# Kernel optimization log

Hardware: AMD Instinct MI355X
Metric: run time of the kernel (lower is better)

Reference implementation:

```python
import jax, jax.numpy as jnp
import numpy as np
from jax import lax

T = 256          # sentence length
WD, TD = 300, 100  # word/tag embedding dims
H = WD + TD      # LSTM hidden (=input) size, per module __init__
VOCAB, NTAGS = 50000, 50
MLP_H = 400


def setup_inputs() -> dict:
    key = jax.random.key(0)
    ks = jax.random.split(key, 20)
    s = 0.05  # small init scale for numerical stability
    return {
        "words": jax.random.randint(ks[0], (T,), 0, VOCAB),
        "tags": jax.random.randint(ks[1], (T,), 0, NTAGS),
        "word_emb": jax.random.normal(ks[2], (VOCAB, WD), jnp.float32),
        "tag_emb": jax.random.normal(ks[3], (NTAGS, TD), jnp.float32),
        "Wih0": jax.random.normal(ks[4], (2, 4 * H, H), jnp.float32) * s,
        "Whh0": jax.random.normal(ks[5], (2, 4 * H, H), jnp.float32) * s,
        "bih0": jax.random.normal(ks[6], (2, 4 * H), jnp.float32) * s,
        "bhh0": jax.random.normal(ks[7], (2, 4 * H), jnp.float32) * s,
        "Wih1": jax.random.normal(ks[8], (2, 4 * H, 2 * H), jnp.float32) * s,
        "Whh1": jax.random.normal(ks[9], (2, 4 * H, H), jnp.float32) * s,
        "bih1": jax.random.normal(ks[10], (2, 4 * H), jnp.float32) * s,
        "bhh1": jax.random.normal(ks[11], (2, 4 * H), jnp.float32) * s,
        "W1": jax.random.normal(ks[12], (MLP_H, 4 * H), jnp.float32) * s,
        "b1": jax.random.normal(ks[13], (MLP_H,), jnp.float32) * s,
        "W2": jax.random.normal(ks[14], (1, MLP_H), jnp.float32) * s,
        "b2": jax.random.normal(ks[15], (1,), jnp.float32) * s,
        "h0": jax.random.normal(ks[16], (2, 2, H), jnp.float32),  # [layer, dir, H]
        "c0": jax.random.normal(ks[17], (2, 2, H), jnp.float32),
    }


def _lstm_dir(xs, Wih, Whh, bih, bhh, h0, c0, reverse):
    # xs: [T, D]; torch LSTM gate order i, f, g, o
    def step(carry, xt):
        h, c = carry
        g = xt @ Wih.T + bih + h @ Whh.T + bhh  # [4H]
        i, f, gg, o = jnp.split(g, 4)
        c = jax.nn.sigmoid(f) * c + jax.nn.sigmoid(i) * jnp.tanh(gg)
        h = jax.nn.sigmoid(o) * jnp.tanh(c)
        return (h, c), h
    _, hs = lax.scan(step, (h0, c0), xs, reverse=reverse)
    return hs  # [T, H]


def _forward(words, tags, word_emb, tag_emb, Wih0, Whh0, bih0, bhh0,
             Wih1, Whh1, bih1, bhh1, W1, b1, W2, b2, h0, c0):
    x = jnp.concatenate([word_emb[words], tag_emb[tags]], axis=1)  # [T, H]
    # layer 0, both directions
    hf0 = _lstm_dir(x, Wih0[0], Whh0[0], bih0[0], bhh0[0], h0[0, 0], c0[0, 0], False)
    hb0 = _lstm_dir(x, Wih0[1], Whh0[1], bih0[1], bhh0[1], h0[0, 1], c0[0, 1], True)
    x1 = jnp.concatenate([hf0, hb0], axis=1)  # [T, 2H]
    # layer 1
    hf1 = _lstm_dir(x1, Wih1[0], Whh1[0], bih1[0], bhh1[0], h0[1, 0], c0[1, 0], False)
    hb1 = _lstm_dir(x1, Wih1[1], Whh1[1], bih1[1], bhh1[1], h0[1, 1], c0[1, 1], True)
    hvec = jnp.concatenate([hf1, hb1], axis=1)  # [T, 2H]
    # batched pairwise MLP: score(i,j) = W2 @ tanh(W1 @ [h_i; h_j] + b1) + b2
    # Split W1 so the concat is never materialized over all T^2 pairs.
    W1a, W1b = W1[:, :2 * H], W1[:, 2 * H:]
    pi = hvec @ W1a.T  # [T, MLP_H] contribution of head word i
    pj = hvec @ W1b.T  # [T, MLP_H] contribution of dependent word j
    act = jnp.tanh(pi[:, None, :] + pj[None, :, :] + b1)  # [T, T, MLP_H]
    scores = act @ W2[0] + b2[0]  # [T, T]
    # diagonal stays 0 (permutations exclude i == j; scoreTensor was zeroed)
    return scores * (1.0 - jnp.eye(T, dtype=scores.dtype))


def reference(words, tags, word_emb, tag_emb, Wih0, Whh0, bih0, bhh0,
              Wih1, Whh1, bih1, bhh1, W1, b1, W2, b2, h0, c0):
    return _forward(words, tags, word_emb, tag_emb, Wih0, Whh0, bih0, bhh0,
                    Wih1, Whh1, bih1, bhh1, W1, b1, W2, b2, h0, c0)
```

## Files before the change

kernel.cpp:

```cpp
#include <hip/hip_runtime.h>
#include <hip/hip_bf16.h>

#define T 256
#define H 400
#define G4 1600
#define WD 300
#define TD 100
#define MLP_H 400
#define NBLK_D 25
#define HB 16
#define GR 64
#define WSTR 202
#define NPAIR 200

typedef _Float16 f16;
typedef _Float16 half2t __attribute__((ext_vector_type(2)));
typedef unsigned long long u64;
typedef unsigned int u32;

__device__ __forceinline__ float fexp(float x) {
    return __builtin_amdgcn_exp2f(x * 1.4426950408889634f);
}
__device__ __forceinline__ float sigf(float x) {
    return __builtin_amdgcn_rcpf(1.0f + fexp(-x));
}
__device__ __forceinline__ float tanhf_fast(float x) {
    return 1.0f - 2.0f * __builtin_amdgcn_rcpf(1.0f + fexp(2.0f * x));
}
__device__ __forceinline__ unsigned short f16bits(f16 x) {
    union { f16 h; unsigned short u; } v; v.h = x; return v.u;
}
__device__ __forceinline__ u32 packh2(float a, float b) {
    half2t hv; hv.x = (_Float16)a; hv.y = (_Float16)b;
    return __builtin_bit_cast(u32, hv);
}

#if __has_builtin(__builtin_amdgcn_fdot2)
__device__ __forceinline__ float dot2u(u32 a, u32 b, float c) {
    return __builtin_amdgcn_fdot2(__builtin_bit_cast(half2t, a),
                                  __builtin_bit_cast(half2t, b), c, false);
}
#else
__device__ __forceinline__ float dot2u(u32 a, u32 b, float c) {
    half2t x = __builtin_bit_cast(half2t, a), y = __builtin_bit_cast(half2t, b);
    return fmaf((float)x.y, (float)y.y, fmaf((float)x.x, (float)y.x, c));
}
#endif

__device__ __forceinline__ u64 sysload(const u64* p) {
    return __hip_atomic_load(p, __ATOMIC_RELAXED, __HIP_MEMORY_SCOPE_SYSTEM);
}
__device__ __forceinline__ void sysstore(u64* p, u64 v) {
    __hip_atomic_store(p, v, __ATOMIC_RELAXED, __HIP_MEMORY_SCOPE_SYSTEM);
}

__global__ void gather_k(const int* __restrict__ words, const int* __restrict__ tags,
                         const float* __restrict__ wemb, const float* __restrict__ temb,
                         float* __restrict__ x0) {
    int t = blockIdx.x;
    int w = words[t], g = tags[t];
    for (int c = threadIdx.x; c < H; c += 128) {
        float v = (c < WD) ? wemb[w * WD + c] : temb[g * TD + (c - WD)];
        x0[t * H + c] = v;
    }
}

__global__ __launch_bounds__(256) void gemm_tn(
    const float* __restrict__ X, int ldx,
    const float* __restrict__ Wt, int ldw, int wofs,
    const float* __restrict__ bias1, const float* __restrict__ bias2,
    float* __restrict__ out, int ldo, int Rt, int K) {
    __shared__ float Xs[64][17];
    __shared__ float Ws[64][17];
    const int tid = threadIdx.x;
    const int t0 = blockIdx.x * 64, r0 = blockIdx.y * 64;
    const int lr = tid >> 2, kq = (tid & 3) * 4;
    const int ti = tid >> 4, rj = tid & 15;
    float acc[4][4] = {};
    for (int k0 = 0; k0 < K; k0 += 16) {
        float4 xv = *(const float4*)(X + (size_t)(t0 + lr) * ldx + k0 + kq);
        Xs[lr][kq + 0] = xv.x; Xs[lr][kq + 1] = xv.y;
        Xs[lr][kq + 2] = xv.z; Xs[lr][kq + 3] = xv.w;
        int r = r0 + lr;
        float4 wv = make_float4(0.f, 0.f, 0.f, 0.f);
        if (r < Rt) wv = *(const float4*)(Wt + (size_t)r * ldw + wofs + k0 + kq);
        Ws[lr][kq + 0] = wv.x; Ws[lr][kq + 1] = wv.y;
        Ws[lr][kq + 2] = wv.z; Ws[lr][kq + 3] = wv.w;
        __syncthreads();
#pragma unroll
        for (int k = 0; k < 16; k++) {
            float xr[4], wr[4];
#pragma unroll
            for (int m = 0; m < 4; m++) xr[m] = Xs[ti * 4 + m][k];
#pragma unroll
            for (int n = 0; n < 4; n++) wr[n] = Ws[rj * 4 + n][k];
#pragma unroll
            for (int m = 0; m < 4; m++)
#pragma unroll
                for (int n = 0; n < 4; n++)
                    acc[m][n] = fmaf(xr[m], wr[n], acc[m][n]);
        }
        __syncthreads();
    }
    int rq = r0 + rj * 4;
    if (rq < Rt) {
        float b[4];
#pragma unroll
        for (int n = 0; n < 4; n++) {
            int r = rq + n;
            b[n] = (bias1 ? bias1[r] : 0.f) + (bias2 ? bias2[r] : 0.f);
        }
#pragma unroll
        for (int m = 0; m < 4; m++) {
            int t = t0 + ti * 4 + m;
            float4 o;
            o.x = acc[m][0] + b[0]; o.y = acc[m][1] + b[1];
            o.z = acc[m][2] + b[2]; o.w = acc[m][3] + b[3];
            *(float4*)(out + (size_t)t * ldo + rq) = o;
        }
    }
}

__global__ void lstm_init5(const float* __restrict__ h0, u64* sA, u64* sB) {
    int tid = threadIdx.x;
    const int TOT = 2 * 2 * NPAIR;
    for (int i = tid; i < TOT; i += 256) { sA[i] = 0xFFFFULL; sB[i] = 0xFFFFULL; }
    __syncthreads();
    for (int p = tid; p < 2 * NPAIR; p += 256) {
        int d = p / NPAIR, pr = p - d * NPAIR;
        size_t off = (size_t)(d * 2 + 0) * NPAIR + pr;
        f16 a0 = (f16)h0[d * H + 2 * pr], b0 = (f16)h0[d * H + 2 * pr + 1];
        sA[off] = 0ULL | ((u64)f16bits(a0) << 16) | ((u64)f16bits(b0) << 32);
        f16 a1 = (f16)h0[2 * H + d * H + 2 * pr], b1 = (f16)h0[2 * H + d * H + 2 * pr + 1];
        sB[off] = 0ULL | ((u64)f16bits(a1) << 16) | ((u64)f16bits(b1) << 32);
    }
}

__global__ __launch_bounds__(512, 1) void lstm_layer8(
    const float* __restrict__ G,
    const float* __restrict__ Whh,
    const float* __restrict__ c0l,
    float* __restrict__ xout,
    u64* __restrict__ slots) {
    const int role = blockIdx.x;
    const int dir = role / NBLK_D, blk = role - dir * NBLK_D;
    const int tid = threadIdx.x;
    const float* Wd = Whh + (size_t)dir * G4 * H;
    const float* Gd = G + (size_t)dir * T * G4;
    u64* sd = slots + (size_t)dir * 2 * NPAIR;

    __shared__ u32 wlds[GR * WSTR];
    __shared__ __align__(16) u32 hsh[NPAIR];
    __shared__ float gsum[GR];
    __shared__ float gsh[2][GR];

    for (int idx = tid; idx < GR * 100; idx += 512) {
        int row = idx / 100, c4 = idx - row * 100;
        int g = row >> 4, r = row & 15;
        const float4* src = (const float4*)(Wd + (size_t)(g * H + blk * HB + r) * H);
        float4 f = src[c4];
        *(uint2*)&wlds[row * WSTR + c4 * 2] =
            make_uint2(packh2(f.x, f.y), packh2(f.z, f.w));
    }
    if (tid >= 448) {
        int i = tid - 448, gg = i >> 4, rr = i & 15;
        int tt0 = dir ? (T - 1) : 0;
        gsh[0][i] = Gd[(size_t)tt0 * G4 + gg * H + blk * HB + rr];
    } else if (tid < 8) {
        u64 v = sysload(sd + blk * 8 + tid);
        hsh[blk * 8 + tid] = (u32)(v >> 16);
    }
    float c = (tid < 64) ? c0l[dir * H + blk * HB + (tid & 15)] : 0.f;
    __syncthreads();

#pragma clang loop unroll(disable)
    for (int s = 0; s < T; ++s) {
        if (tid >= 256 && tid < 448) {
            int f = tid - 256;
            int widx = f + (f >= blk * 8 ? 8 : 0);
            u64* src = sd + (size_t)(s & 1) * NPAIR + widx;
            u64 v = sysload(src);
            int spins = 0;
            while ((unsigned)(v & 0xFFFFULL) != (unsigned)s) {
                if (++spins > 16384) {
                    v = __hip_atomic_fetch_add(src, 0ULL, __ATOMIC_RELAXED,
                                               __HIP_MEMORY_SCOPE_AGENT);
                } else {
                    v = sysload(src);
                }
            }
            hsh[widx] = (u32)(v >> 16);
        } else if (tid >= 448) {
            int sn = (s + 1 < T) ? (s + 1) : s;
            int tt = dir ? (T - 1 - sn) : sn;
            int i = tid - 448, gg = i >> 4, rr = i & 15;
            gsh[(s + 1) & 1][i] = Gd[(size_t)tt * G4 + gg * H + blk * HB + rr];
        }
        __syncthreads();

        if (tid < 256) {
            const int row = tid >> 2, sl = tid & 3;
            const u32* wp = &wlds[row * WSTR + sl * 50];
            const u32* hp = &hsh[sl * 50];
            float a0 = 0.f, a1 = 0.f, a2 = 0.f, a3 = 0.f;
#pragma unroll
            for (int i = 0; i < 12; ++i) {
                uint2 wv0 = *(const uint2*)&wp[4 * i];
                uint2 hv0 = *(const uint2*)&hp[4 * i];
                uint2 wv1 = *(const uint2*)&wp[4 * i + 2];
                uint2 hv1 = *(const uint2*)&hp[4 * i + 2];
                a0 = dot2u(wv0.x, hv0.x, a0);
                a1 = dot2u(wv0.y, hv0.y, a1);
                a2 = dot2u(wv1.x, hv1.x, a2);
                a3 = dot2u(wv1.y, hv1.y, a3);
            }
            {
                uint2 wv = *(const uint2*)&wp[48];
                uint2 hv = *(const uint2*)&hp[48];
                a0 = dot2u(wv.x, hv.x, a0);
                a1 = dot2u(wv.y, hv.y, a1);
            }
            float a = (a0 + a1) + (a2 + a3);
            a += __shfl_xor(a, 1);
            a += __shfl_xor(a, 2);
            if (sl == 0) gsum[row] = a;
        }
        __syncthreads();

        if (tid < 64) {
            const int r = tid & 15;
            const float* gc = gsh[s & 1];
            float iv = gsum[r]      + gc[r];
            float fv = gsum[16 + r] + gc[16 + r];
            float gv = gsum[32 + r] + gc[32 + r];
            float ov = gsum[48 + r] + gc[48 + r];
            float cn = sigf(fv) * c + sigf(iv) * tanhf_fast(gv);
            c = cn;
            float hn = sigf(ov) * tanhf_fast(cn);
            u32 hb = (u32)f16bits((f16)hn);
            u32 lo = __shfl(hb, (2 * tid) & 63);
            u32 hi = __shfl(hb, (2 * tid + 1) & 63);
            if (tid < 8) {
                u32 pk = (lo & 0xFFFFu) | (hi << 16);
                hsh[blk * 8 + tid] = pk;
                sysstore(sd + (size_t)((s + 1) & 1) * NPAIR + blk * 8 + tid,
                         (u64)(unsigned)(s + 1) | ((u64)pk << 16));
            }
            const int tt = dir ? (T - 1 - s) : s;
            if (tid < 16)
                xout[(size_t)tt * (2 * H) + dir * H + blk * HB + tid] = hn;
        }
    }
}

__global__ __launch_bounds__(256) void scores_k(
    const float* __restrict__ pi, const float* __restrict__ pj,
    const float* __restrict__ w2, const float* __restrict__ b2p,
    float* __restrict__ out) {
    __shared__ float Ps[16][401];
    __shared__ float Qs[16][401];
    __shared__ float w2s[400];
    const int tid = threadIdx.x;
    const int i0 = blockIdx.y * 16, j0 = blockIdx.x * 16;
    for (int r = 0; r < 16; r++) {
        for (int k = tid; k < MLP_H; k += 256) {
            Ps[r][k] = pi[(size_t)(i0 + r) * MLP_H + k];
            Qs[r][k] = pj[(size_t)(j0 + r) * MLP_H + k];
        }
    }
    for (int k = tid; k < MLP_H; k += 256) w2s[k] = w2[k];
    __syncthreads();
    const int ti = tid >> 4, tj = tid & 15;
    float acc = 0.f;
#pragma unroll 4
    for (int k = 0; k < MLP_H; k++) {
        float x = Ps[ti][k] + Qs[tj][k];
        acc = fmaf(w2s[k], tanhf_fast(x), acc);
    }
    const int i = i0 + ti, j = j0 + tj;
    out[(size_t)i * T + j] = (i == j) ? 0.f : (acc + b2p[0]);
}

extern "C" void kernel_launch(void* const* d_in, const int* in_sizes, int n_in,
                              void* d_out, int out_size, void* d_ws, size_t ws_size,
                              hipStream_t stream) {
    const int*   words = (const int*)d_in[0];
    const int*   tags  = (const int*)d_in[1];
    const float* wemb  = (const float*)d_in[2];
    const float* temb  = (const float*)d_in[3];
    const float* Wih0  = (const float*)d_in[4];
    const float* Whh0  = (const float*)d_in[5];
    const float* bih0  = (const float*)d_in[6];
    const float* bhh0  = (const float*)d_in[7];
    const float* Wih1  = (const float*)d_in[8];
    const float* Whh1  = (const float*)d_in[9];
    const float* bih1  = (const float*)d_in[10];
    const float* bhh1  = (const float*)d_in[11];
    const float* W1    = (const float*)d_in[12];
    const float* b1    = (const float*)d_in[13];
    const float* W2    = (const float*)d_in[14];
    const float* b2    = (const float*)d_in[15];
    const float* h0    = (const float*)d_in[16];
    const float* c0    = (const float*)d_in[17];
    float* out = (float*)d_out;

    float* W = (float*)d_ws;
    float* x0   = W;
    float* x1   = W + 102400;
    float* hvec = W + 307200;
    float* Gb   = W + 512000;
    float* pi   = W + 1331200;
    float* pj   = W + 1433600;
    u64* slotsA = (u64*)W;
    u64* slotsB = (u64*)(W + 2048);

    gather_k<<<T, 128, 0, stream>>>(words, tags, wemb, temb, x0);

    for (int d = 0; d < 2; d++) {
        gemm_tn<<<dim3(4, 25), 256, 0, stream>>>(
            x0, H, Wih0 + (size_t)d * G4 * H, H, 0,
            bih0 + d * G4, bhh0 + d * G4,
            Gb + (size_t)d * T * G4, G4, G4, H);
    }
    lstm_init5<<<1, 256, 0, stream>>>(h0, slotsA, slotsB);
    lstm_layer8<<<2 * NBLK_D, 512, 0, stream>>>(Gb, Whh0, c0, x1, slotsA);

    for (int d = 0; d < 2; d++) {
        gemm_tn<<<dim3(4, 25), 256, 0, stream>>>(
            x1, 2 * H, Wih1 + (size_t)d * G4 * (2 * H), 2 * H, 0,
            bih1 + d * G4, bhh1 + d * G4,
            Gb + (size_t)d * T * G4, G4, G4, 2 * H);
    }
    lstm_layer8<<<2 * NBLK_D, 512, 0, stream>>>(Gb, Whh1, c0 + 2 * H, hvec, slotsB);

    gemm_tn<<<dim3(4, 7), 256, 0, stream>>>(
        hvec, 2 * H, W1, G4, 0, b1, nullptr, pi, MLP_H, MLP_H, 2 * H);
    gemm_tn<<<dim3(4, 7), 256, 0, stream>>>(
        hvec, 2 * H, W1, G4, 2 * H, nullptr, nullptr, pj, MLP_H, MLP_H, 2 * H);

    scores_k<<<dim3(16, 16), 256, 0, stream>>>(pi, pj, W2, b2, out);
}
```

Before: 1.439 ms.

## Remap LSTM recurrence so each wavefront owns its gates and drops a barrier

Restructures the per-step recurrent kernel so that each 64-lane wavefront holds all four gates for four hidden units. The reduction and cell update then happen inside one wavefront through shuffles, which removes the second __syncthreads and the shared gsum round trip. The h vector is double-buffered by step parity and the G prefetch is triple-buffered, so a single barrier per step is safe. The weight layout becomes per-thread contiguous chunks with padded strides to suit 128-bit h loads. All 256 worker threads now run the activation math redundantly, where 64 did before.

```diff
diff --git a/kernel.cpp b/kernel.cpp
--- a/kernel.cpp
+++ b/kernel.cpp
@@ -9,9 +9,8 @@
 #define MLP_H 400
 #define NBLK_D 25
 #define HB 16
-#define GR 64
-#define WSTR 202
 #define NPAIR 200
+#define CSTR 51
 
 typedef _Float16 f16;
 typedef _Float16 half2t __attribute__((ext_vector_type(2)));
@@ -136,7 +135,7 @@
     }
 }
 
-__global__ __launch_bounds__(512, 1) void lstm_layer8(
+__global__ __launch_bounds__(512, 1) void lstm_layer11(
     const float* __restrict__ G,
     const float* __restrict__ Whh,
     const float* __restrict__ c0l,
@@ -149,107 +148,123 @@
     const float* Gd = G + (size_t)dir * T * G4;
     u64* sd = slots + (size_t)dir * 2 * NPAIR;
 
-    __shared__ u32 wlds[GR * WSTR];
-    __shared__ __align__(16) u32 hsh[NPAIR];
-    __shared__ float gsum[GR];
-    __shared__ float gsh[2][GR];
-
-    for (int idx = tid; idx < GR * 100; idx += 512) {
-        int row = idx / 100, c4 = idx - row * 100;
-        int g = row >> 4, r = row & 15;
-        const float4* src = (const float4*)(Wd + (size_t)(g * H + blk * HB + r) * H);
-        float4 f = src[c4];
-        *(uint2*)&wlds[row * WSTR + c4 * 2] =
-            make_uint2(packh2(f.x, f.y), packh2(f.z, f.w));
-    }
-    if (tid >= 448) {
+    __shared__ u32 wlds[256 * CSTR];
+    __shared__ __align__(16) u32 hsh[2][4 * 52];
+    __shared__ float gsh[3][64];
+
+    const bool worker = tid < 256;
+    const int v = tid >> 6;
+    const int l = tid & 63;
+    const int hr = l & 3;
+    const int gate = (l >> 2) & 3;
+    const int sl = l >> 4;
+
+    if (worker) {
+        const int row = gate * H + blk * HB + v * 4 + hr;
+        const float4* src = (const float4*)(Wd + (size_t)row * H + sl * 100);
+        u32* chunk = &wlds[tid * CSTR];
+#pragma unroll
+        for (int m = 0; m < 25; ++m) {
+            float4 f = src[m];
+            chunk[2 * m]     = packh2(f.x, f.y);
+            chunk[2 * m + 1] = packh2(f.z, f.w);
+        }
+    }
+    float c = c0l[dir * H + blk * HB + (worker ? v * 4 + hr : 0)];
+
+    if (tid < 16) {
+        int par = tid >> 3, rem = tid & 7;
+        hsh[par][(rem >> 1) * 52 + 50 + (rem & 1)] = 0u;
+    } else if (tid >= 16 && tid < 24) {
+        int p = blk * 8 + (tid - 16);
+        u64 x = sysload(sd + p);
+        hsh[0][(p / 50) * 52 + p % 50] = (u32)(x >> 16);
+    } else if (tid >= 448) {
         int i = tid - 448, gg = i >> 4, rr = i & 15;
         int tt0 = dir ? (T - 1) : 0;
         gsh[0][i] = Gd[(size_t)tt0 * G4 + gg * H + blk * HB + rr];
-    } else if (tid < 8) {
-        u64 v = sysload(sd + blk * 8 + tid);
-        hsh[blk * 8 + tid] = (u32)(v >> 16);
-    }
-    float c = (tid < 64) ? c0l[dir * H + blk * HB + (tid & 15)] : 0.f;
-    __syncthreads();
-
+    }
+
+    int widx = 0, hix = 0;
+    if (tid >= 256 && tid < 448) {
+        int f = tid - 256;
+        widx = f + (f >= blk * 8 ? 8 : 0);
+        hix = (widx / 50) * 52 + widx % 50;
+    }
+    const int pubp = blk * 8 + v * 2 + l;
+    const int pubix = (pubp / 50) * 52 + pubp % 50;
+
+    int rd3 = 0;
 #pragma clang loop unroll(disable)
     for (int s = 0; s < T; ++s) {
-        if (tid >= 256 && tid < 448) {
-            int f = tid - 256;
-            int widx = f + (f >= blk * 8 ? 8 : 0);
-            u64* src = sd + (size_t)(s & 1) * NPAIR + widx;
-            u64 v = sysload(src);
-            int spins = 0;
-            while ((unsigned)(v & 0xFFFFULL) != (unsigned)s) {
-                if (++spins > 16384) {
-                    v = __hip_atomic_fetch_add(src, 0ULL, __ATOMIC_RELAXED,
-                                               __HIP_MEMORY_SCOPE_AGENT);
-                } else {
-                    v = sysload(src);
+        const int wr3 = (rd3 == 2) ? 0 : rd3 + 1;
+        if (tid >= 256) {
+            if (tid < 448) {
+                u64* src = sd + (size_t)(s & 1) * NPAIR + widx;
+                u64 x = sysload(src);
+                int spins = 0;
+                while ((unsigned)(x & 0xFFFFULL) != (unsigned)s) {
+                    if (++spins > 16384) {
+                        x = __hip_atomic_fetch_add(src, 0ULL, __ATOMIC_RELAXED,
+                                                   __HIP_MEMORY_SCOPE_AGENT);
+                    } else {
+                        x = sysload(src);
+                    }
                 }
+                hsh[s & 1][hix] = (u32)(x >> 16);
+            } else {
+                int sn = (s + 1 < T) ? (s + 1) : s;
+                int tt = dir ? (T - 1 - sn) : sn;
+                int i = tid - 448, gg = i >> 4, rr = i & 15;
+                gsh[wr3][i] = Gd[(size_t)tt * G4 + gg * H + blk * HB + rr];
             }
-            hsh[widx] = (u32)(v >> 16);
-        } else if (tid >= 448) {
-            int sn = (s + 1 < T) ? (s + 1) : s;
-            int tt = dir ? (T - 1 - sn) : sn;
-            int i = tid - 448, gg = i >> 4, rr = i & 15;
-            gsh[(s + 1) & 1][i] = Gd[(size_t)tt * G4 + gg * H + blk * HB + rr];
         }
         __syncthreads();
 
-        if (tid < 256) {
-            const int row = tid >> 2, sl = tid & 3;
-            const u32* wp = &wlds[row * WSTR + sl * 50];
-            const u32* hp = &hsh[sl * 50];
+        if (worker) {
+            const u32* wp = &wlds[tid * CSTR];
+            const uint4* hp = (const uint4*)&hsh[s & 1][sl * 52];
             float a0 = 0.f, a1 = 0.f, a2 = 0.f, a3 = 0.f;
 #pragma unroll
             for (int i = 0; i < 12; ++i) {
-                uint2 wv0 = *(const uint2*)&wp[4 * i];
-                uint2 hv0 = *(const uint2*)&hp[4 * i];
-                uint2 wv1 = *(const uint2*)&wp[4 * i + 2];
-                uint2 hv1 = *(const uint2*)&hp[4 * i + 2];
-                a0 = dot2u(wv0.x, hv0.x, a0);
-                a1 = dot2u(wv0.y, hv0.y, a1);
-                a2 = dot2u(wv1.x, hv1.x, a2);
-                a3 = dot2u(wv1.y, hv1.y, a3);
+                uint4 q = hp[i];
+                a0 = dot2u(wp[4 * i + 0], q.x, a0);
+                a1 = dot2u(wp[4 * i + 1], q.y, a1);
+                a2 = dot2u(wp[4 * i + 2], q.z, a2);
+                a3 = dot2u(wp[4 * i + 3], q.w, a3);
             }
             {
-                uint2 wv = *(const uint2*)&wp[48];
-                uint2 hv = *(const uint2*)&hp[48];
-                a0 = dot2u(wv.x, hv.x, a0);
-                a1 = dot2u(wv.y, hv.y, a1);
+                uint4 q = hp[12];
+                a0 = dot2u(wp[48], q.x, a0);
+                a1 = dot2u(wp[49], q.y, a1);
             }
             float a = (a0 + a1) + (a2 + a3);
-            a += __shfl_xor(a, 1);
-            a += __shfl_xor(a, 2);
-            if (sl == 0) gsum[row] = a;
-        }
-        __syncthreads();
-
-        if (tid < 64) {
-            const int r = tid & 15;
-            const float* gc = gsh[s & 1];
-            float iv = gsum[r]      + gc[r];
-            float fv = gsum[16 + r] + gc[16 + r];
-            float gv = gsum[32 + r] + gc[32 + r];
-            float ov = gsum[48 + r] + gc[48 + r];
+            a += __shfl_xor(a, 16);
+            a += __shfl_xor(a, 32);
+            float iv = __shfl(a, hr);
+            float fv = __shfl(a, hr + 4);
+            float gv = __shfl(a, hr + 8);
+            float ov = __shfl(a, hr + 12);
+            const float* gc = gsh[rd3];
+            const int lr = v * 4 + hr;
+            iv += gc[lr]; fv += gc[16 + lr]; gv += gc[32 + lr]; ov += gc[48 + lr];
             float cn = sigf(fv) * c + sigf(iv) * tanhf_fast(gv);
             c = cn;
             float hn = sigf(ov) * tanhf_fast(cn);
             u32 hb = (u32)f16bits((f16)hn);
-            u32 lo = __shfl(hb, (2 * tid) & 63);
-            u32 hi = __shfl(hb, (2 * tid + 1) & 63);
-            if (tid < 8) {
+            u32 lo = __shfl(hb, (2 * l) & 63);
+            u32 hi = __shfl(hb, (2 * l + 1) & 63);
+            const int tt = dir ? (T - 1 - s) : s;
+            if (l < 2) {
                 u32 pk = (lo & 0xFFFFu) | (hi << 16);
-                hsh[blk * 8 + tid] = pk;
-                sysstore(sd + (size_t)((s + 1) & 1) * NPAIR + blk * 8 + tid,
+                hsh[(s + 1) & 1][pubix] = pk;
+                sysstore(sd + (size_t)((s + 1) & 1) * NPAIR + pubp,
                          (u64)(unsigned)(s + 1) | ((u64)pk << 16));
             }
-            const int tt = dir ? (T - 1 - s) : s;
-            if (tid < 16)
-                xout[(size_t)tt * (2 * H) + dir * H + blk * HB + tid] = hn;
-        }
+            if (l < 4)
+                xout[(size_t)tt * (2 * H) + dir * H + blk * HB + lr] = hn;
+        }
+        rd3 = wr3;
     }
 }
 
@@ -323,7 +338,7 @@
             Gb + (size_t)d * T * G4, G4, G4, H);
     }
     lstm_init5<<<1, 256, 0, stream>>>(h0, slotsA, slotsB);
-    lstm_layer8<<<2 * NBLK_D, 512, 0, stream>>>(Gb, Whh0, c0, x1, slotsA);
+    lstm_layer11<<<2 * NBLK_D, 512, 0, stream>>>(Gb, Whh0, c0, x1, slotsA);
 
     for (int d = 0; d < 2; d++) {
         gemm_tn<<<dim3(4, 25), 256, 0, stream>>>(
@@ -331,7 +346,7 @@
             bih1 + d * G4, bhh1 + d * G4,
             Gb + (size_t)d * T * G4, G4, G4, 2 * H);
     }
-    lstm_layer8<<<2 * NBLK_D, 512, 0, stream>>>(Gb, Whh1, c0 + 2 * H, hvec, slotsB);
+    lstm_layer11<<<2 * NBLK_D, 512, 0, stream>>>(Gb, Whh1, c0 + 2 * H, hvec, slotsB);
 
     gemm_tn<<<dim3(4, 7), 256, 0, stream>>>(
         hvec, 2 * H, W1, G4, 0, b1, nullptr, pi, MLP_H, MLP_H, 2 * H);
```

Result: slower. 1.630 ms (+13.3%).
